# Performance work log

Hardware: AMD Instinct MI355X
Metric: run time of the kernel (lower is better)

The kernel has to match this reference:

```python
import jax, jax.numpy as jnp
import numpy as np

MARGIN = 0.3
NORM = 2.0  # p-norm used by both pairwise() and PairwiseDistance

M, C = 65536, 256   # n*h*w pixels, feature channels
K, P, Q = 20, 2048, 2048  # classes 1..nclass-1, positives, negatives per class


def setup_inputs() -> dict:
    key = jax.random.key(0)
    k1, k2, k3 = jax.random.split(key, 3)
    features = jax.random.normal(k1, (M, C), dtype=jnp.float32)
    pos_idx = jax.random.randint(k2, (K, P), 0, M)
    neg_idx = jax.random.randint(k3, (K, Q), 0, M)
    return {"features": features, "pos_idx": pos_idx, "neg_idx": neg_idx}


def _pairwise(x, y):
    # torch: clamp(xx - 2xy + yy, 0); (dis + eps) ** (1/norm)
    eps = 0.0001 / x.shape[1]
    xx = jnp.sum(x * x, axis=1)           # [P]
    yy = jnp.sum(y * y, axis=1)           # [Q]
    xy = x @ y.T                           # [P,Q] GEMM
    dis = jnp.clip(xx[:, None] - 2.0 * xy + yy[None, :], 0.0)
    return (dis + eps) ** (1.0 / NORM)


def _pdist(x1, x2):
    # PairwiseDistance: (clamp(sum(|x1-x2|^p), 0) + eps) ** (1/p)
    eps = 0.0001 / x1.shape[1]
    out = jnp.sum(jnp.abs(x1 - x2) ** NORM, axis=1)
    return (jnp.clip(out, 0.0) + eps) ** (1.0 / NORM)


def _class_loss(pos, neg):
    # hard mining on detached features (indices only, as in generate_triplet_simple)
    pos_d = jax.lax.stop_gradient(pos)
    neg_d = jax.lax.stop_gradient(neg)
    hp = jnp.argmax(_pairwise(pos_d, pos_d), axis=1)   # hardest positive per anchor
    hn = jnp.argmin(_pairwise(pos_d, neg_d), axis=1)   # hardest negative per anchor
    d_p = _pdist(pos, pos[hp])
    d_n = _pdist(pos, neg[hn])
    return jnp.mean(jnp.clip(MARGIN + d_p - d_n, 0.0))


def reference(features, pos_idx, neg_idx):
    f = jax.nn.sigmoid(features)          # torch.sigmoid(features)
    pos = f[pos_idx]                      # [K,P,C]
    neg = f[neg_idx]                      # [K,Q,C]
    losses = jax.vmap(_class_loss)(pos, neg)  # per-class triplet losses
    return jnp.sum(losses)                # loss accumulated over classes
```

## Files before the change

### kernel.cpp

```cpp
#include <hip/hip_runtime.h>
#include <stdint.h>

#define M_ROWS 65536
#define C_DIM  256
#define K_CLS  20
#define P_POS  2048
#define MARGIN_F 0.3f
#define EPS_D (0.0001f / 256.0f)
#define SCALE1 0x7F7F7F7Fu
#define SCALE2 0x80808080u

typedef float floatx4 __attribute__((ext_vector_type(4)));
typedef int   intx8   __attribute__((ext_vector_type(8)));
union Frag8 { intx8 v; uint4 q[2]; };

__device__ __forceinline__ void async_copy16(const void* g, void* l) {
    __builtin_amdgcn_global_load_lds(
        (const __attribute__((address_space(1))) void*)g,
        (__attribute__((address_space(3))) void*)l, 16, 0, 0);
}
__device__ __forceinline__ float sigm(float x) { return 1.f / (1.f + __expf(-x)); }

__device__ __forceinline__ void negA(Frag8& f) {
#pragma unroll
    for (int t = 0; t < 8; ++t) f.v[t] ^= (int)0x80808080u;
}

#define VMCNT2() asm volatile("s_waitcnt vmcnt(2)" ::: "memory")
#define VMCNT0() asm volatile("s_waitcnt vmcnt(0)" ::: "memory")

__global__ __launch_bounds__(256) void sigmoid_norm_k(
        const float* __restrict__ feat,
        unsigned int* __restrict__ S8,
        float* __restrict__ xx,
        unsigned int* __restrict__ hp,
        unsigned int* __restrict__ hn,
        float* __restrict__ out) {
    {
        const int idx = blockIdx.x * 256 + threadIdx.x;
        if (idx < K_CLS * P_POS) { hp[idx] = 0u; hn[idx] = 0xFFFFFFFFu; }
        if (idx == 0) out[0] = 0.f;
    }
    const int wave = threadIdx.x >> 6, lane = threadIdx.x & 63;
    const int row = blockIdx.x * 4 + wave;
    const float4 v = *(const float4*)(feat + (size_t)row * C_DIM + lane * 4);

    const int p01 = __builtin_amdgcn_cvt_pk_fp8_f32(sigm(v.x), sigm(v.y), 0, false);
    const int p23 = __builtin_amdgcn_cvt_pk_fp8_f32(sigm(v.z), sigm(v.w), 0, false);
    const unsigned int packed = (unsigned int)(p01 & 0xFFFF) | ((unsigned int)p23 << 16);
    S8[(size_t)row * 64 + lane] = packed;

    const float q0 = __builtin_amdgcn_cvt_f32_fp8(p01, 0);
    const float q1 = __builtin_amdgcn_cvt_f32_fp8(p01, 1);
    const float q2 = __builtin_amdgcn_cvt_f32_fp8(p23, 0);
    const float q3 = __builtin_amdgcn_cvt_f32_fp8(p23, 1);
    float sum = q0 * q0 + q1 * q1 + q2 * q2 + q3 * q3;
#pragma unroll
    for (int off = 32; off; off >>= 1) sum += __shfl_down(sum, off);
    if (lane == 0) xx[row] = sum;
}

__global__ __launch_bounds__(256, 3) void select_k(
        const unsigned int* __restrict__ S8,
        const float* __restrict__ xx,
        const int* __restrict__ pos_idx,
        const int* __restrict__ neg_idx,
        unsigned int* __restrict__ hp,
        unsigned int* __restrict__ hn) {
    __shared__ __align__(16) uint4 Bt4[3][512];
    __shared__ float yyL[512];

    const int tid    = threadIdx.x;
    const int w      = tid >> 6;
    const int lane   = tid & 63;
    const int lane15 = lane & 15;
    const int quad   = lane >> 4;

    const int bid    = blockIdx.x;
    const int ctid   = bid % 40;
    const int rest   = bid / 40;
    const int i_blk  = rest >> 2;
    const int jq     = rest & 3;
    const int k      = ctid >> 1;
    const int isNeg  = ctid & 1;
    const int i0     = i_blk * 256;
    const int j0     = jq * 512;

    const int* __restrict__ idxA = pos_idx + k * P_POS;
    const int* __restrict__ idxB = (isNeg ? neg_idx : pos_idx) + k * P_POS;
    unsigned int* outKey         = (isNeg ? hn : hp) + k * P_POS;

    const char* S8B = (const char*)S8;

    const int rl  = lane >> 4;
    const int cch = lane & 15;
    int rloc[2], soff[2];
#pragma unroll
    for (int c = 0; c < 2; ++c) {
        rloc[c] = (w * 2 + c) * 4 + rl;
        soff[c] = (cch ^ (rloc[c] & 15)) << 4;
    }

    uint32_t g_pk[16];
#pragma unroll
    for (int t = 0; t < 16; ++t) {
        const uint32_t a0 = (uint32_t)idxB[j0 + t * 32 + rloc[0]];
        const uint32_t a1 = (uint32_t)idxB[j0 + t * 32 + rloc[1]];
        g_pk[t] = (a0 & 0xFFFFu) | (a1 << 16);
    }

#pragma unroll
    for (int t = 0; t < 2; ++t) {
        const int jj = t * 256 + tid;
        yyL[jj] = xx[idxB[j0 + jj]];
    }

    Frag8 A_reg[4][2];
#pragma unroll
    for (int si = 0; si < 4; ++si) {
        const int gi = idxA[i0 + w * 64 + si * 16 + lane15];
        const char* rb = S8B + ((size_t)(uint32_t)gi << 8) + quad * 32;
#pragma unroll
        for (int s = 0; s < 2; ++s) {
            A_reg[si][s].q[0] = *(const uint4*)(rb + s * 128);
            A_reg[si][s].q[1] = *(const uint4*)(rb + s * 128 + 16);
            negA(A_reg[si][s]);
        }
    }

    const int bidx0 = lane15 * 16 + ((quad * 2) ^ lane15);

    float bestv[16];
    const float binit = isNeg ? 3.4e38f : -3.4e38f;
#pragma unroll
    for (int t = 0; t < 16; ++t) bestv[t] = binit;

#pragma unroll
    for (int t = 0; t < 2; ++t) {
        char* lb = (char*)Bt4[t] + (w * 2) * 1024;
        async_copy16(S8B + ((size_t)(g_pk[t] & 0xFFFFu) << 8) + soff[0], lb);
        async_copy16(S8B + ((size_t)(g_pk[t] >> 16) << 8) + soff[1], lb + 1024);
    }

    __syncthreads();

#pragma unroll
    for (int jc = 0; jc < 16; ++jc) {
        if (jc) {
            if (jc == 15) VMCNT0(); else VMCNT2();
            __builtin_amdgcn_s_barrier();
            __builtin_amdgcn_sched_barrier(0);
        }

        const float yv0 = yyL[(jc << 5) + lane15];
        const float yv1 = yyL[(jc << 5) + 16 + lane15];

        if (jc < 14) {
            const uint32_t pk = g_pk[jc + 2];
            char* lb = (char*)Bt4[(jc + 2) % 3] + (w * 2) * 1024;
            async_copy16(S8B + ((size_t)(pk & 0xFFFFu) << 8) + soff[0], lb);
            async_copy16(S8B + ((size_t)(pk >> 16) << 8) + soff[1], lb + 1024);
        }

        const floatx4 yv4_0 = {yv0, yv0, yv0, yv0};
        const floatx4 yv4_1 = {yv1, yv1, yv1, yv1};
        floatx4 acc[2][4];
        {
            Frag8 bf0, bf1;
            bf0.q[0] = Bt4[jc % 3][bidx0];
            bf0.q[1] = Bt4[jc % 3][bidx0 ^ 1];
            bf1.q[0] = Bt4[jc % 3][bidx0 + 256];
            bf1.q[1] = Bt4[jc % 3][(bidx0 ^ 1) + 256];
#pragma unroll
            for (int si = 0; si < 4; ++si)
                acc[0][si] = __builtin_amdgcn_mfma_scale_f32_16x16x128_f8f6f4(
                    A_reg[si][0].v, bf0.v, yv4_0, 0, 0,
                    0, SCALE2, 0, SCALE1);
#pragma unroll
            for (int si = 0; si < 4; ++si)
                acc[1][si] = __builtin_amdgcn_mfma_scale_f32_16x16x128_f8f6f4(
                    A_reg[si][0].v, bf1.v, yv4_1, 0, 0,
                    0, SCALE2, 0, SCALE1);
        }
        {
            Frag8 bf0, bf1;
            bf0.q[0] = Bt4[jc % 3][bidx0 ^ 8];
            bf0.q[1] = Bt4[jc % 3][bidx0 ^ 9];
            bf1.q[0] = Bt4[jc % 3][(bidx0 ^ 8) + 256];
            bf1.q[1] = Bt4[jc % 3][(bidx0 ^ 9) + 256];
#pragma unroll
            for (int si = 0; si < 4; ++si)
                acc[0][si] = __builtin_amdgcn_mfma_scale_f32_16x16x128_f8f6f4(
                    A_reg[si][1].v, bf0.v, acc[0][si], 0, 0,
                    0, SCALE2, 0, SCALE1);
#pragma unroll
            for (int si = 0; si < 4; ++si)
                acc[1][si] = __builtin_amdgcn_mfma_scale_f32_16x16x128_f8f6f4(
                    A_reg[si][1].v, bf1.v, acc[1][si], 0, 0,
                    0, SCALE2, 0, SCALE1);
        }

        const uint32_t jb0 = (uint32_t)((j0 + (jc << 5)) | lane15);
        const uint32_t jb1 = jb0 | 16u;
#pragma unroll
        for (int si = 0; si < 4; ++si)
#pragma unroll
            for (int r = 0; r < 4; ++r) {
                const float e0 = __uint_as_float(
                    (__float_as_uint(acc[0][si][r]) & 0xFFFFF800u) | jb0);
                const float e1 = __uint_as_float(
                    (__float_as_uint(acc[1][si][r]) & 0xFFFFF800u) | jb1);
                const int slot = si * 4 + r;
                bestv[slot] = isNeg ? fminf(fminf(bestv[slot], e0), e1)
                                    : fmaxf(fmaxf(bestv[slot], e0), e1);
            }
    }

#pragma unroll
    for (int slot = 0; slot < 16; ++slot) {
#pragma unroll
        for (int off = 1; off < 16; off <<= 1) {
            const float ov = __shfl_xor(bestv[slot], off);
            bestv[slot] = isNeg ? fminf(bestv[slot], ov) : fmaxf(bestv[slot], ov);
        }
    }
    if (lane15 == 0) {
#pragma unroll
        for (int si = 0; si < 4; ++si)
#pragma unroll
            for (int r = 0; r < 4; ++r) {
                const int row = w * 64 + si * 16 + quad * 4 + r;
                const uint32_t u = __float_as_uint(bestv[si * 4 + r]);
                const uint32_t key = (u & 0x80000000u) ? ~u : (u | 0x80000000u);
                if (isNeg) atomicMin(&outKey[i0 + row], key);
                else       atomicMax(&outKey[i0 + row], key);
            }
    }
}

#define ACC16(UA, UP, UN)                                                     \
    {                                                                         \
        float xa, d;                                                          \
        xa = __builtin_amdgcn_cvt_f32_fp8((int)(UA), 0);                      \
        d = xa - __builtin_amdgcn_cvt_f32_fp8((int)(UP), 0); dp += d * d;     \
        d = xa - __builtin_amdgcn_cvt_f32_fp8((int)(UN), 0); dn += d * d;     \
        xa = __builtin_amdgcn_cvt_f32_fp8((int)(UA), 1);                      \
        d = xa - __builtin_amdgcn_cvt_f32_fp8((int)(UP), 1); dp += d * d;     \
        d = xa - __builtin_amdgcn_cvt_f32_fp8((int)(UN), 1); dn += d * d;     \
        xa = __builtin_amdgcn_cvt_f32_fp8((int)(UA), 2);                      \
        d = xa - __builtin_amdgcn_cvt_f32_fp8((int)(UP), 2); dp += d * d;     \
        d = xa - __builtin_amdgcn_cvt_f32_fp8((int)(UN), 2); dn += d * d;     \
        xa = __builtin_amdgcn_cvt_f32_fp8((int)(UA), 3);                      \
        d = xa - __builtin_amdgcn_cvt_f32_fp8((int)(UP), 3); dp += d * d;     \
        d = xa - __builtin_amdgcn_cvt_f32_fp8((int)(UN), 3); dn += d * d;     \
    }

__global__ __launch_bounds__(256) void loss_k(
        const unsigned int* __restrict__ S8,
        const int* __restrict__ pos_idx,
        const int* __restrict__ neg_idx,
        const unsigned int* __restrict__ hp,
        const unsigned int* __restrict__ hn,
        float* __restrict__ terms) {
    const int tid    = threadIdx.x;
    const int lane15 = tid & 15;
    const int grp    = tid >> 4;
    const int a      = blockIdx.x * 16 + grp;
    const int k      = a >> 11;
    const int i      = a & 2047;
    const int* pidx = pos_idx + (k << 11);
    const int* nidx = neg_idx + (k << 11);
    const unsigned int kp = hp[a], kn = hn[a];
    const int jp = (int)((kp & 0x80000000u) ? (kp & 2047u) : ((~kp) & 2047u));
    const int jn = (int)((kn & 0x80000000u) ? (kn & 2047u) : ((~kn) & 2047u));
    const int ga = pidx[i];
    const int gp = pidx[jp];
    const int gn = nidx[jn];

    const char* S8B = (const char*)S8;
    const uint4 va = *(const uint4*)(S8B + ((size_t)(uint32_t)ga << 8) + lane15 * 16);
    const uint4 vp = *(const uint4*)(S8B + ((size_t)(uint32_t)gp << 8) + lane15 * 16);
    const uint4 vn = *(const uint4*)(S8B + ((size_t)(uint32_t)gn << 8) + lane15 * 16);

    float dp = 0.f, dn = 0.f;
    ACC16(va.x, vp.x, vn.x)
    ACC16(va.y, vp.y, vn.y)
    ACC16(va.z, vp.z, vn.z)
    ACC16(va.w, vp.w, vn.w)

#pragma unroll
    for (int off = 1; off < 16; off <<= 1) {
        dp += __shfl_xor(dp, off);
        dn += __shfl_xor(dn, off);
    }
    if (lane15 == 0) {
        const float d_p = sqrtf(fmaxf(dp, 0.f) + EPS_D);
        const float d_n = sqrtf(fmaxf(dn, 0.f) + EPS_D);
        terms[a] = fmaxf(MARGIN_F + d_p - d_n, 0.f);
    }
}

__global__ __launch_bounds__(1024) void reduce_k(
        const float* __restrict__ terms, float* __restrict__ out) {
    __shared__ float red[1024];
    const int tid = threadIdx.x;
    red[tid] = terms[blockIdx.x * 1024 + tid];
    __syncthreads();
    for (int off = 512; off; off >>= 1) {
        if (tid < off) red[tid] += red[tid + off];
        __syncthreads();
    }
    if (tid == 0) atomicAdd(out, red[0] * (1.0f / (float)P_POS));
}

extern "C" void kernel_launch(void* const* d_in, const int* in_sizes, int n_in,
                              void* d_out, int out_size, void* d_ws, size_t ws_size,
                              hipStream_t stream) {
    const float* feat    = (const float*)d_in[0];
    const int*   pos_idx = (const int*)d_in[1];
    const int*   neg_idx = (const int*)d_in[2];

    char* ws = (char*)d_ws;
    unsigned int* S8 = (unsigned int*)ws;
    float*        xx = (float*)(ws + 16777216);
    unsigned int* hp = (unsigned int*)(ws + 17039360);
    unsigned int* hn = (unsigned int*)(ws + 17203200);
    float*     terms = (float*)(ws + 17367040);

    sigmoid_norm_k<<<M_ROWS / 4, 256, 0, stream>>>(feat, S8, xx, hp, hn,
                                                   (float*)d_out);

    select_k<<<32 * 40, 256, 0, stream>>>(S8, xx, pos_idx, neg_idx, hp, hn);

    loss_k<<<(K_CLS * P_POS) / 16, 256, 0, stream>>>(S8, pos_idx, neg_idx, hp, hn, terms);

    reduce_k<<<40, 1024, 0, stream>>>(terms, (float*)d_out);
}
```

Baseline: 161.8 us.

## Fuse all four stages into one persistent kernel with grid-wide barriers

Replaces the four separate launches (sigmoid/quantize, hard-mining GEMM, loss, reduce) with a single persistent kernel of 640 blocks. The stages are separated by atomic-counter grid barriers, and the final reduction is done by block 0 after a counter wait. This removes launch gaps and the intermediate terms buffer. In exchange it depends on all 640 blocks being co-resident, which the 3-blocks-per-CU launch bound is meant to guarantee, and it adds spin-wait barriers plus a memset launch.

```diff
diff --git a/kernel.cpp b/kernel.cpp
--- a/kernel.cpp
+++ b/kernel.cpp
@@ -9,6 +9,7 @@
 #define EPS_D (0.0001f / 256.0f)
 #define SCALE1 0x7F7F7F7Fu
 #define SCALE2 0x80808080u
+#define GRID_N 640u
 
 typedef float floatx4 __attribute__((ext_vector_type(4)));
 typedef int   intx8   __attribute__((ext_vector_type(8)));
@@ -29,213 +30,18 @@
 #define VMCNT2() asm volatile("s_waitcnt vmcnt(2)" ::: "memory")
 #define VMCNT0() asm volatile("s_waitcnt vmcnt(0)" ::: "memory")
 
-__global__ __launch_bounds__(256) void sigmoid_norm_k(
-        const float* __restrict__ feat,
-        unsigned int* __restrict__ S8,
-        float* __restrict__ xx,
-        unsigned int* __restrict__ hp,
-        unsigned int* __restrict__ hn,
-        float* __restrict__ out) {
-    {
-        const int idx = blockIdx.x * 256 + threadIdx.x;
-        if (idx < K_CLS * P_POS) { hp[idx] = 0u; hn[idx] = 0xFFFFFFFFu; }
-        if (idx == 0) out[0] = 0.f;
-    }
-    const int wave = threadIdx.x >> 6, lane = threadIdx.x & 63;
-    const int row = blockIdx.x * 4 + wave;
-    const float4 v = *(const float4*)(feat + (size_t)row * C_DIM + lane * 4);
-
-    const int p01 = __builtin_amdgcn_cvt_pk_fp8_f32(sigm(v.x), sigm(v.y), 0, false);
-    const int p23 = __builtin_amdgcn_cvt_pk_fp8_f32(sigm(v.z), sigm(v.w), 0, false);
-    const unsigned int packed = (unsigned int)(p01 & 0xFFFF) | ((unsigned int)p23 << 16);
-    S8[(size_t)row * 64 + lane] = packed;
-
-    const float q0 = __builtin_amdgcn_cvt_f32_fp8(p01, 0);
-    const float q1 = __builtin_amdgcn_cvt_f32_fp8(p01, 1);
-    const float q2 = __builtin_amdgcn_cvt_f32_fp8(p23, 0);
-    const float q3 = __builtin_amdgcn_cvt_f32_fp8(p23, 1);
-    float sum = q0 * q0 + q1 * q1 + q2 * q2 + q3 * q3;
-#pragma unroll
-    for (int off = 32; off; off >>= 1) sum += __shfl_down(sum, off);
-    if (lane == 0) xx[row] = sum;
-}
-
-__global__ __launch_bounds__(256, 3) void select_k(
-        const unsigned int* __restrict__ S8,
-        const float* __restrict__ xx,
-        const int* __restrict__ pos_idx,
-        const int* __restrict__ neg_idx,
-        unsigned int* __restrict__ hp,
-        unsigned int* __restrict__ hn) {
-    __shared__ __align__(16) uint4 Bt4[3][512];
-    __shared__ float yyL[512];
-
-    const int tid    = threadIdx.x;
-    const int w      = tid >> 6;
-    const int lane   = tid & 63;
-    const int lane15 = lane & 15;
-    const int quad   = lane >> 4;
-
-    const int bid    = blockIdx.x;
-    const int ctid   = bid % 40;
-    const int rest   = bid / 40;
-    const int i_blk  = rest >> 2;
-    const int jq     = rest & 3;
-    const int k      = ctid >> 1;
-    const int isNeg  = ctid & 1;
-    const int i0     = i_blk * 256;
-    const int j0     = jq * 512;
-
-    const int* __restrict__ idxA = pos_idx + k * P_POS;
-    const int* __restrict__ idxB = (isNeg ? neg_idx : pos_idx) + k * P_POS;
-    unsigned int* outKey         = (isNeg ? hn : hp) + k * P_POS;
-
-    const char* S8B = (const char*)S8;
-
-    const int rl  = lane >> 4;
-    const int cch = lane & 15;
-    int rloc[2], soff[2];
-#pragma unroll
-    for (int c = 0; c < 2; ++c) {
-        rloc[c] = (w * 2 + c) * 4 + rl;
-        soff[c] = (cch ^ (rloc[c] & 15)) << 4;
-    }
-
-    uint32_t g_pk[16];
-#pragma unroll
-    for (int t = 0; t < 16; ++t) {
-        const uint32_t a0 = (uint32_t)idxB[j0 + t * 32 + rloc[0]];
-        const uint32_t a1 = (uint32_t)idxB[j0 + t * 32 + rloc[1]];
-        g_pk[t] = (a0 & 0xFFFFu) | (a1 << 16);
-    }
-
-#pragma unroll
-    for (int t = 0; t < 2; ++t) {
-        const int jj = t * 256 + tid;
-        yyL[jj] = xx[idxB[j0 + jj]];
-    }
-
-    Frag8 A_reg[4][2];
-#pragma unroll
-    for (int si = 0; si < 4; ++si) {
-        const int gi = idxA[i0 + w * 64 + si * 16 + lane15];
-        const char* rb = S8B + ((size_t)(uint32_t)gi << 8) + quad * 32;
-#pragma unroll
-        for (int s = 0; s < 2; ++s) {
-            A_reg[si][s].q[0] = *(const uint4*)(rb + s * 128);
-            A_reg[si][s].q[1] = *(const uint4*)(rb + s * 128 + 16);
-            negA(A_reg[si][s]);
-        }
-    }
-
-    const int bidx0 = lane15 * 16 + ((quad * 2) ^ lane15);
-
-    float bestv[16];
-    const float binit = isNeg ? 3.4e38f : -3.4e38f;
-#pragma unroll
-    for (int t = 0; t < 16; ++t) bestv[t] = binit;
-
-#pragma unroll
-    for (int t = 0; t < 2; ++t) {
-        char* lb = (char*)Bt4[t] + (w * 2) * 1024;
-        async_copy16(S8B + ((size_t)(g_pk[t] & 0xFFFFu) << 8) + soff[0], lb);
-        async_copy16(S8B + ((size_t)(g_pk[t] >> 16) << 8) + soff[1], lb + 1024);
-    }
-
+__device__ __forceinline__ void gsync(unsigned int* c) {
     __syncthreads();
-
-#pragma unroll
-    for (int jc = 0; jc < 16; ++jc) {
-        if (jc) {
-            if (jc == 15) VMCNT0(); else VMCNT2();
-            __builtin_amdgcn_s_barrier();
-            __builtin_amdgcn_sched_barrier(0);
-        }
-
-        const float yv0 = yyL[(jc << 5) + lane15];
-        const float yv1 = yyL[(jc << 5) + 16 + lane15];
-
-        if (jc < 14) {
-            const uint32_t pk = g_pk[jc + 2];
-            char* lb = (char*)Bt4[(jc + 2) % 3] + (w * 2) * 1024;
-            async_copy16(S8B + ((size_t)(pk & 0xFFFFu) << 8) + soff[0], lb);
-            async_copy16(S8B + ((size_t)(pk >> 16) << 8) + soff[1], lb + 1024);
-        }
-
-        const floatx4 yv4_0 = {yv0, yv0, yv0, yv0};
-        const floatx4 yv4_1 = {yv1, yv1, yv1, yv1};
-        floatx4 acc[2][4];
-        {
-            Frag8 bf0, bf1;
-            bf0.q[0] = Bt4[jc % 3][bidx0];
-            bf0.q[1] = Bt4[jc % 3][bidx0 ^ 1];
-            bf1.q[0] = Bt4[jc % 3][bidx0 + 256];
-            bf1.q[1] = Bt4[jc % 3][(bidx0 ^ 1) + 256];
-#pragma unroll
-            for (int si = 0; si < 4; ++si)
-                acc[0][si] = __builtin_amdgcn_mfma_scale_f32_16x16x128_f8f6f4(
-                    A_reg[si][0].v, bf0.v, yv4_0, 0, 0,
-                    0, SCALE2, 0, SCALE1);
-#pragma unroll
-            for (int si = 0; si < 4; ++si)
-                acc[1][si] = __builtin_amdgcn_mfma_scale_f32_16x16x128_f8f6f4(
-                    A_reg[si][0].v, bf1.v, yv4_1, 0, 0,
-                    0, SCALE2, 0, SCALE1);
-        }
-        {
-            Frag8 bf0, bf1;
-            bf0.q[0] = Bt4[jc % 3][bidx0 ^ 8];
-            bf0.q[1] = Bt4[jc % 3][bidx0 ^ 9];
-            bf1.q[0] = Bt4[jc % 3][(bidx0 ^ 8) + 256];
-            bf1.q[1] = Bt4[jc % 3][(bidx0 ^ 9) + 256];
-#pragma unroll
-            for (int si = 0; si < 4; ++si)
-                acc[0][si] = __builtin_amdgcn_mfma_scale_f32_16x16x128_f8f6f4(
-                    A_reg[si][1].v, bf0.v, acc[0][si], 0, 0,
-                    0, SCALE2, 0, SCALE1);
-#pragma unroll
-            for (int si = 0; si < 4; ++si)
-                acc[1][si] = __builtin_amdgcn_mfma_scale_f32_16x16x128_f8f6f4(
-                    A_reg[si][1].v, bf1.v, acc[1][si], 0, 0,
-                    0, SCALE2, 0, SCALE1);
-        }
-
-        const uint32_t jb0 = (uint32_t)((j0 + (jc << 5)) | lane15);
-        const uint32_t jb1 = jb0 | 16u;
-#pragma unroll
-        for (int si = 0; si < 4; ++si)
-#pragma unroll
-            for (int r = 0; r < 4; ++r) {
-                const float e0 = __uint_as_float(
-                    (__float_as_uint(acc[0][si][r]) & 0xFFFFF800u) | jb0);
-                const float e1 = __uint_as_float(
-                    (__float_as_uint(acc[1][si][r]) & 0xFFFFF800u) | jb1);
-                const int slot = si * 4 + r;
-                bestv[slot] = isNeg ? fminf(fminf(bestv[slot], e0), e1)
-                                    : fmaxf(fmaxf(bestv[slot], e0), e1);
-            }
-    }
-
-#pragma unroll
-    for (int slot = 0; slot < 16; ++slot) {
-#pragma unroll
-        for (int off = 1; off < 16; off <<= 1) {
-            const float ov = __shfl_xor(bestv[slot], off);
-            bestv[slot] = isNeg ? fminf(bestv[slot], ov) : fmaxf(bestv[slot], ov);
-        }
-    }
-    if (lane15 == 0) {
-#pragma unroll
-        for (int si = 0; si < 4; ++si)
-#pragma unroll
-            for (int r = 0; r < 4; ++r) {
-                const int row = w * 64 + si * 16 + quad * 4 + r;
-                const uint32_t u = __float_as_uint(bestv[si * 4 + r]);
-                const uint32_t key = (u & 0x80000000u) ? ~u : (u | 0x80000000u);
-                if (isNeg) atomicMin(&outKey[i0 + row], key);
-                else       atomicMax(&outKey[i0 + row], key);
-            }
-    }
+    if (threadIdx.x == 0) {
+        __threadfence();
+        __hip_atomic_fetch_add(c, 1u, __ATOMIC_RELEASE, __HIP_MEMORY_SCOPE_AGENT);
+        while (__hip_atomic_load(c, __ATOMIC_ACQUIRE,
+                                 __HIP_MEMORY_SCOPE_AGENT) < GRID_N) {
+            __builtin_amdgcn_s_sleep(2);
+        }
+        __threadfence();
+    }
+    __syncthreads();
 }
 
 #define ACC16(UA, UP, UN)                                                     \
@@ -255,62 +61,270 @@
         d = xa - __builtin_amdgcn_cvt_f32_fp8((int)(UN), 3); dn += d * d;     \
     }
 
-__global__ __launch_bounds__(256) void loss_k(
-        const unsigned int* __restrict__ S8,
+__global__ __launch_bounds__(256, 3) void fused_k(
+        const float* __restrict__ feat,
+        unsigned int* __restrict__ S8,
+        float* __restrict__ xx,
         const int* __restrict__ pos_idx,
         const int* __restrict__ neg_idx,
-        const unsigned int* __restrict__ hp,
-        const unsigned int* __restrict__ hn,
-        float* __restrict__ terms) {
+        unsigned int* __restrict__ hp,
+        unsigned int* __restrict__ hn,
+        float* __restrict__ partials,
+        unsigned int* __restrict__ bars,
+        float* __restrict__ out) {
+    __shared__ __align__(16) uint4 Bt4[3][512];
+    __shared__ float yyL[512];
+    __shared__ float sm[16];
+
     const int tid    = threadIdx.x;
-    const int lane15 = tid & 15;
-    const int grp    = tid >> 4;
-    const int a      = blockIdx.x * 16 + grp;
-    const int k      = a >> 11;
-    const int i      = a & 2047;
-    const int* pidx = pos_idx + (k << 11);
-    const int* nidx = neg_idx + (k << 11);
-    const unsigned int kp = hp[a], kn = hn[a];
-    const int jp = (int)((kp & 0x80000000u) ? (kp & 2047u) : ((~kp) & 2047u));
-    const int jn = (int)((kn & 0x80000000u) ? (kn & 2047u) : ((~kn) & 2047u));
-    const int ga = pidx[i];
-    const int gp = pidx[jp];
-    const int gn = nidx[jn];
-
-    const char* S8B = (const char*)S8;
-    const uint4 va = *(const uint4*)(S8B + ((size_t)(uint32_t)ga << 8) + lane15 * 16);
-    const uint4 vp = *(const uint4*)(S8B + ((size_t)(uint32_t)gp << 8) + lane15 * 16);
-    const uint4 vn = *(const uint4*)(S8B + ((size_t)(uint32_t)gn << 8) + lane15 * 16);
-
-    float dp = 0.f, dn = 0.f;
-    ACC16(va.x, vp.x, vn.x)
-    ACC16(va.y, vp.y, vn.y)
-    ACC16(va.z, vp.z, vn.z)
-    ACC16(va.w, vp.w, vn.w)
-
-#pragma unroll
-    for (int off = 1; off < 16; off <<= 1) {
-        dp += __shfl_xor(dp, off);
-        dn += __shfl_xor(dn, off);
-    }
-    if (lane15 == 0) {
-        const float d_p = sqrtf(fmaxf(dp, 0.f) + EPS_D);
-        const float d_n = sqrtf(fmaxf(dn, 0.f) + EPS_D);
-        terms[a] = fmaxf(MARGIN_F + d_p - d_n, 0.f);
-    }
-}
-
-__global__ __launch_bounds__(1024) void reduce_k(
-        const float* __restrict__ terms, float* __restrict__ out) {
-    __shared__ float red[1024];
-    const int tid = threadIdx.x;
-    red[tid] = terms[blockIdx.x * 1024 + tid];
+    const int wave   = tid >> 6;
+    const int lane   = tid & 63;
+    const int lane15 = lane & 15;
+    const int quad   = lane >> 4;
+    const char* S8B  = (const char*)S8;
+
+    for (int g = blockIdx.x; g < M_ROWS / 4; g += (int)GRID_N) {
+        const int row = g * 4 + wave;
+        const float4 v = *(const float4*)(feat + (size_t)row * C_DIM + lane * 4);
+        const int p01 = __builtin_amdgcn_cvt_pk_fp8_f32(sigm(v.x), sigm(v.y), 0, false);
+        const int p23 = __builtin_amdgcn_cvt_pk_fp8_f32(sigm(v.z), sigm(v.w), 0, false);
+        S8[(size_t)row * 64 + lane] =
+            (unsigned int)(p01 & 0xFFFF) | ((unsigned int)p23 << 16);
+        const float q0 = __builtin_amdgcn_cvt_f32_fp8(p01, 0);
+        const float q1 = __builtin_amdgcn_cvt_f32_fp8(p01, 1);
+        const float q2 = __builtin_amdgcn_cvt_f32_fp8(p23, 0);
+        const float q3 = __builtin_amdgcn_cvt_f32_fp8(p23, 1);
+        float sum = q0 * q0 + q1 * q1 + q2 * q2 + q3 * q3;
+#pragma unroll
+        for (int off = 32; off; off >>= 1) sum += __shfl_down(sum, off);
+        if (lane == 0) xx[row] = sum;
+    }
+    {
+        const int idx = blockIdx.x * 256 + tid;
+        if (idx < K_CLS * P_POS) { hp[idx] = 0u; hn[idx] = 0xFFFFFFFFu; }
+    }
+    gsync(&bars[0]);
+
+    for (int jj = 0; jj < 2; ++jj) {
+        const int job = (int)blockIdx.x + jj * (int)GRID_N;
+        __syncthreads();
+
+        const int ctid  = job % 40;
+        const int rest  = job / 40;
+        const int i_blk = rest >> 2;
+        const int jq    = rest & 3;
+        const int k     = ctid >> 1;
+        const int isNeg = ctid & 1;
+        const int i0    = i_blk * 256;
+        const int j0    = jq * 512;
+
+        const int* __restrict__ idxA = pos_idx + k * P_POS;
+        const int* __restrict__ idxB = (isNeg ? neg_idx : pos_idx) + k * P_POS;
+        unsigned int* outKey         = (isNeg ? hn : hp) + k * P_POS;
+
+        const int rl  = lane >> 4;
+        const int cch = lane & 15;
+        int rloc[2], soff[2];
+#pragma unroll
+        for (int c = 0; c < 2; ++c) {
+            rloc[c] = (wave * 2 + c) * 4 + rl;
+            soff[c] = (cch ^ (rloc[c] & 15)) << 4;
+        }
+
+        uint32_t g_pk[16];
+#pragma unroll
+        for (int t = 0; t < 16; ++t) {
+            const uint32_t a0 = (uint32_t)idxB[j0 + t * 32 + rloc[0]];
+            const uint32_t a1 = (uint32_t)idxB[j0 + t * 32 + rloc[1]];
+            g_pk[t] = (a0 & 0xFFFFu) | (a1 << 16);
+        }
+#pragma unroll
+        for (int t = 0; t < 2; ++t) {
+            const int jjx = t * 256 + tid;
+            yyL[jjx] = xx[idxB[j0 + jjx]];
+        }
+        Frag8 A_reg[4][2];
+#pragma unroll
+        for (int si = 0; si < 4; ++si) {
+            const int gi = idxA[i0 + wave * 64 + si * 16 + lane15];
+            const char* rb = S8B + ((size_t)(uint32_t)gi << 8) + quad * 32;
+#pragma unroll
+            for (int s = 0; s < 2; ++s) {
+                A_reg[si][s].q[0] = *(const uint4*)(rb + s * 128);
+                A_reg[si][s].q[1] = *(const uint4*)(rb + s * 128 + 16);
+                negA(A_reg[si][s]);
+            }
+        }
+        const int bidx0 = lane15 * 16 + ((quad * 2) ^ lane15);
+
+        float bestv[16];
+        const float binit = isNeg ? 3.4e38f : -3.4e38f;
+#pragma unroll
+        for (int t = 0; t < 16; ++t) bestv[t] = binit;
+
+#pragma unroll
+        for (int t = 0; t < 2; ++t) {
+            char* lb = (char*)Bt4[t] + (wave * 2) * 1024;
+            async_copy16(S8B + ((size_t)(g_pk[t] & 0xFFFFu) << 8) + soff[0], lb);
+            async_copy16(S8B + ((size_t)(g_pk[t] >> 16) << 8) + soff[1], lb + 1024);
+        }
+        __syncthreads();
+
+#pragma unroll
+        for (int jc = 0; jc < 16; ++jc) {
+            if (jc) {
+                if (jc == 15) VMCNT0(); else VMCNT2();
+                __builtin_amdgcn_s_barrier();
+                __builtin_amdgcn_sched_barrier(0);
+            }
+            const float yv0 = yyL[(jc << 5) + lane15];
+            const float yv1 = yyL[(jc << 5) + 16 + lane15];
+
+            if (jc < 14) {
+                const uint32_t pk = g_pk[jc + 2];
+                char* lb = (char*)Bt4[(jc + 2) % 3] + (wave * 2) * 1024;
+                async_copy16(S8B + ((size_t)(pk & 0xFFFFu) << 8) + soff[0], lb);
+                async_copy16(S8B + ((size_t)(pk >> 16) << 8) + soff[1], lb + 1024);
+            }
+
+            const floatx4 yv4_0 = {yv0, yv0, yv0, yv0};
+            const floatx4 yv4_1 = {yv1, yv1, yv1, yv1};
+            floatx4 acc[2][4];
+            {
+                Frag8 bf0, bf1;
+                bf0.q[0] = Bt4[jc % 3][bidx0];
+                bf0.q[1] = Bt4[jc % 3][bidx0 ^ 1];
+                bf1.q[0] = Bt4[jc % 3][bidx0 + 256];
+                bf1.q[1] = Bt4[jc % 3][(bidx0 ^ 1) + 256];
+#pragma unroll
+                for (int si = 0; si < 4; ++si)
+                    acc[0][si] = __builtin_amdgcn_mfma_scale_f32_16x16x128_f8f6f4(
+                        A_reg[si][0].v, bf0.v, yv4_0, 0, 0, 0, SCALE2, 0, SCALE1);
+#pragma unroll
+                for (int si = 0; si < 4; ++si)
+                    acc[1][si] = __builtin_amdgcn_mfma_scale_f32_16x16x128_f8f6f4(
+                        A_reg[si][0].v, bf1.v, yv4_1, 0, 0, 0, SCALE2, 0, SCALE1);
+            }
+            {
+                Frag8 bf0, bf1;
+                bf0.q[0] = Bt4[jc % 3][bidx0 ^ 8];
+                bf0.q[1] = Bt4[jc % 3][bidx0 ^ 9];
+                bf1.q[0] = Bt4[jc % 3][(bidx0 ^ 8) + 256];
+                bf1.q[1] = Bt4[jc % 3][(bidx0 ^ 9) + 256];
+#pragma unroll
+                for (int si = 0; si < 4; ++si)
+                    acc[0][si] = __builtin_amdgcn_mfma_scale_f32_16x16x128_f8f6f4(
+                        A_reg[si][1].v, bf0.v, acc[0][si], 0, 0, 0, SCALE2, 0, SCALE1);
+#pragma unroll
+                for (int si = 0; si < 4; ++si)
+                    acc[1][si] = __builtin_amdgcn_mfma_scale_f32_16x16x128_f8f6f4(
+                        A_reg[si][1].v, bf1.v, acc[1][si], 0, 0, 0, SCALE2, 0, SCALE1);
+            }
+
+            const uint32_t jb0 = (uint32_t)((j0 + (jc << 5)) | lane15);
+            const uint32_t jb1 = jb0 | 16u;
+#pragma unroll
+            for (int si = 0; si < 4; ++si)
+#pragma unroll
+                for (int r = 0; r < 4; ++r) {
+                    const float e0 = __uint_as_float(
+                        (__float_as_uint(acc[0][si][r]) & 0xFFFFF800u) | jb0);
+                    const float e1 = __uint_as_float(
+                        (__float_as_uint(acc[1][si][r]) & 0xFFFFF800u) | jb1);
+                    const int slot = si * 4 + r;
+                    bestv[slot] = isNeg ? fminf(fminf(bestv[slot], e0), e1)
+                                        : fmaxf(fmaxf(bestv[slot], e0), e1);
+                }
+        }
+
+#pragma unroll
+        for (int slot = 0; slot < 16; ++slot) {
+#pragma unroll
+            for (int off = 1; off < 16; off <<= 1) {
+                const float ov = __shfl_xor(bestv[slot], off);
+                bestv[slot] = isNeg ? fminf(bestv[slot], ov) : fmaxf(bestv[slot], ov);
+            }
+        }
+        if (lane15 == 0) {
+#pragma unroll
+            for (int si = 0; si < 4; ++si)
+#pragma unroll
+                for (int r = 0; r < 4; ++r) {
+                    const int row = wave * 64 + si * 16 + quad * 4 + r;
+                    const uint32_t u = __float_as_uint(bestv[si * 4 + r]);
+                    const uint32_t key = (u & 0x80000000u) ? ~u : (u | 0x80000000u);
+                    if (isNeg) atomicMin(&outKey[i0 + row], key);
+                    else       atomicMax(&outKey[i0 + row], key);
+                }
+        }
+    }
+    gsync(&bars[1]);
+
+    const int grp = tid >> 4;
+    float lsum = 0.f;
+    for (int c = 0; c < 4; ++c) {
+        const int a = ((int)blockIdx.x * 4 + c) * 16 + grp;
+        const int k = a >> 11;
+        const int i = a & 2047;
+        const int* pidx = pos_idx + (k << 11);
+        const int* nidx = neg_idx + (k << 11);
+        const unsigned int kp = hp[a], kn = hn[a];
+        const int jp = (int)((kp & 0x80000000u) ? (kp & 2047u) : ((~kp) & 2047u));
+        const int jn = (int)((kn & 0x80000000u) ? (kn & 2047u) : ((~kn) & 2047u));
+        const int ga = pidx[i];
+        const int gp = pidx[jp];
+        const int gn = nidx[jn];
+        const uint4 va = *(const uint4*)(S8B + ((size_t)(uint32_t)ga << 8) + lane15 * 16);
+        const uint4 vp = *(const uint4*)(S8B + ((size_t)(uint32_t)gp << 8) + lane15 * 16);
+        const uint4 vn = *(const uint4*)(S8B + ((size_t)(uint32_t)gn << 8) + lane15 * 16);
+        float dp = 0.f, dn = 0.f;
+        ACC16(va.x, vp.x, vn.x)
+        ACC16(va.y, vp.y, vn.y)
+        ACC16(va.z, vp.z, vn.z)
+        ACC16(va.w, vp.w, vn.w)
+#pragma unroll
+        for (int off = 1; off < 16; off <<= 1) {
+            dp += __shfl_xor(dp, off);
+            dn += __shfl_xor(dn, off);
+        }
+        if (lane15 == 0) {
+            const float d_p = sqrtf(fmaxf(dp, 0.f) + EPS_D);
+            const float d_n = sqrtf(fmaxf(dn, 0.f) + EPS_D);
+            lsum += fmaxf(MARGIN_F + d_p - d_n, 0.f);
+        }
+    }
     __syncthreads();
-    for (int off = 512; off; off >>= 1) {
-        if (tid < off) red[tid] += red[tid + off];
-        __syncthreads();
-    }
-    if (tid == 0) atomicAdd(out, red[0] * (1.0f / (float)P_POS));
+    if ((tid & 15) == 0) sm[grp] = lsum;
+    __syncthreads();
+    if (tid == 0) {
+        float s = 0.f;
+#pragma unroll
+        for (int g = 0; g < 16; ++g) s += sm[g];
+        partials[blockIdx.x] = s;
+        __threadfence();
+        __hip_atomic_fetch_add(&bars[2], 1u, __ATOMIC_RELEASE,
+                               __HIP_MEMORY_SCOPE_AGENT);
+    }
+
+    if (blockIdx.x == 0) {
+        if (tid == 0) {
+            while (__hip_atomic_load(&bars[2], __ATOMIC_ACQUIRE,
+                                     __HIP_MEMORY_SCOPE_AGENT) < GRID_N) {
+                __builtin_amdgcn_s_sleep(2);
+            }
+            __threadfence();
+        }
+        __syncthreads();
+        float s = 0.f;
+        for (int i = tid; i < (int)GRID_N; i += 256) s += partials[i];
+#pragma unroll
+        for (int off = 32; off; off >>= 1) s += __shfl_down(s, off);
+        __syncthreads();
+        if (lane == 0) sm[wave] = s;
+        __syncthreads();
+        if (tid == 0)
+            out[0] = (sm[0] + sm[1] + sm[2] + sm[3]) * (1.0f / (float)P_POS);
+    }
 }
 
 extern "C" void kernel_launch(void* const* d_in, const int* in_sizes, int n_in,
@@ -325,14 +339,10 @@
     float*        xx = (float*)(ws + 16777216);
     unsigned int* hp = (unsigned int*)(ws + 17039360);
     unsigned int* hn = (unsigned int*)(ws + 17203200);
-    float*     terms = (float*)(ws + 17367040);
-
-    sigmoid_norm_k<<<M_ROWS / 4, 256, 0, stream>>>(feat, S8, xx, hp, hn,
-                                                   (float*)d_out);
-
-    select_k<<<32 * 40, 256, 0, stream>>>(S8, xx, pos_idx, neg_idx, hp, hn);
-
-    loss_k<<<(K_CLS * P_POS) / 16, 256, 0, stream>>>(S8, pos_idx, neg_idx, hp, hn, terms);
-
-    reduce_k<<<40, 1024, 0, stream>>>(terms, (float*)d_out);
-}
+    float*  partials = (float*)(ws + 17367040);
+    unsigned int* bars = (unsigned int*)(ws + 17369600);
+
+    hipMemsetAsync(bars, 0, 16, stream);
+    fused_k<<<GRID_N, 256, 0, stream>>>(feat, S8, xx, pos_idx, neg_idx,
+                                        hp, hn, partials, bars, (float*)d_out);
+}
```

Result: slower. 429.1 us (+165.2%).
